# Optimization experiments

Hardware: AMD Instinct MI355X
Metric: run time of the kernel (lower is better)

The kernel has to match this reference:

```python
import jax, jax.numpy as jnp
import numpy as np

N_EVENTS = 16384   # original pixel events
D = 128            # input_size
H = 128            # hidden_size
K = 9              # kernel 3x3 -> patch coords
S = 2048           # number of patch sequences
LMAX = 108         # max sequence length
T = 147456         # total patch events = sum(lengths) = 9 * N_EVENTS


def setup_inputs() -> dict:
    key = jax.random.key(0)
    ks = jax.random.split(key, 8)
    events = jax.random.normal(ks[0], (N_EVENTS, D), jnp.float32)
    pos_id = jax.random.randint(ks[1], (T,), 0, K, dtype=jnp.int32)
    orig_event_idx = jax.random.randint(ks[2], (T,), 0, N_EVENTS, dtype=jnp.int32)
    # alternating 36/108 lengths: 1024*36 + 1024*108 = 147456 = T
    lengths = jnp.where(jnp.arange(S) % 2 == 0, 36, 108).astype(jnp.int32)
    std = float(np.sqrt(2.0 / (D + H)))
    scatter_w = jax.random.normal(ks[3], (K, H, D), jnp.float32) * std
    gather_w = jax.random.normal(ks[4], (K, H, H), jnp.float32) * std
    lstm_std = float(1.0 / np.sqrt(H))
    w_ih = jax.random.uniform(ks[5], (4 * H, H), jnp.float32, -lstm_std, lstm_std)
    w_hh = jax.random.uniform(ks[6], (4 * H, H), jnp.float32, -lstm_std, lstm_std)
    ln_g = jnp.ones((H,), jnp.float32)
    ln_b = jnp.zeros((H,), jnp.float32)
    return dict(events=events, scatter_w=scatter_w, gather_w=gather_w,
                w_ih=w_ih, w_hh=w_hh, ln_g=ln_g, ln_b=ln_b,
                pos_id=pos_id, orig_event_idx=orig_event_idx, lengths=lengths)


def _pos_proj(x, W, pos_id):
    # position-indexed projection: out[t] = W[pos_id[t]] @ x[t]
    # loop over small fixed K=9 with masked accumulate (matches the torch loop)
    out = jnp.zeros((x.shape[0], W.shape[1]), x.dtype)
    for k in range(W.shape[0]):
        out = out + jnp.where((pos_id == k)[:, None], x @ W[k].T, 0.0)
    return out


def reference(events, scatter_w, gather_w, w_ih, w_hh, ln_g, ln_b,
              pos_id, orig_event_idx, lengths):
    # scatter events to patch replicas
    x = events[orig_event_idx]                           # [T, D]
    x = _pos_proj(x, scatter_w, pos_id)                  # [T, H]

    # flat (sequence-major) -> padded [S, LMAX, H]
    seq_offsets = jnp.cumsum(lengths) - lengths          # [S]
    seq_ids = jnp.repeat(jnp.arange(S), lengths, total_repeat_length=T)
    pos_in_seq = jnp.arange(T) - seq_offsets[seq_ids]
    padded = jnp.zeros((S, LMAX, H), x.dtype).at[seq_ids, pos_in_seq].set(x)

    # single-layer bias-free LSTM (pytorch gate order i, f, g, o), zero init.
    # zero-padding after each sequence's valid region leaves valid outputs
    # identical to a PackedSequence LSTM.
    def step(carry, xt):                                 # xt: [S, H]
        h, c = carry
        gates = xt @ w_ih.T + h @ w_hh.T                 # [S, 4H]
        i, f, g, o = jnp.split(gates, 4, axis=-1)
        c = jax.nn.sigmoid(f) * c + jax.nn.sigmoid(i) * jnp.tanh(g)
        h = jax.nn.sigmoid(o) * jnp.tanh(c)
        return (h, c), h

    init = (jnp.zeros((S, H), x.dtype), jnp.zeros((S, H), x.dtype))
    _, hs = jax.lax.scan(step, init, jnp.swapaxes(padded, 0, 1))  # [LMAX, S, H]
    o_flat = jnp.swapaxes(hs, 0, 1)[seq_ids, pos_in_seq]          # [T, H]

    o_flat = _pos_proj(o_flat, gather_w, pos_id)                  # [T, H]

    # gather patch events back to pixel events (scatter-add) + residual + LN
    out = jnp.zeros((N_EVENTS, H), x.dtype).at[orig_event_idx].add(o_flat)
    out = out + events                                   # input_proj is None (D == H)
    mu = jnp.mean(out, axis=-1, keepdims=True)
    var = jnp.var(out, axis=-1, keepdims=True)
    out = (out - mu) * jax.lax.rsqrt(var + 1e-5) * ln_g + ln_b
    return out
```

## Files before the change

### kernel.cpp

```cpp
#include <hip/hip_runtime.h>

#define N_EVENTS 16384
#define DIM 128
#define NK 9
#define NSEQ 2048
#define TT 147456
#define CHUNK 64
#define NCHUNK_MAX (TT/CHUNK + NK)
#define NHBLK 576

typedef __attribute__((ext_vector_type(8))) short bf16x8;
typedef __attribute__((ext_vector_type(4))) float f32x4;
typedef __attribute__((ext_vector_type(4))) int i32x4;
typedef __attribute__((ext_vector_type(2))) int i32x2;

#define OFF_EV     0UL
#define OFF_WC     (OFF_EV   + (size_t)N_EVENTS*DIM*2)
#define OFF_SCAT   (OFF_WC   + (size_t)512*256*2)
#define OFF_GATH   (OFF_SCAT + (size_t)NK*DIM*DIM*2)
#define OFF_XS     (OFF_GATH + (size_t)NK*DIM*DIM*2)
#define OFF_HS     (OFF_XS   + (size_t)TT*DIM*2)
#define OFF_KLIST  (OFF_HS   + (size_t)TT*DIM*2)
#define OFF_ECNT   (OFF_KLIST+ (size_t)TT*4)
#define OFF_EOFF   (OFF_ECNT + 16384UL*4)
#define OFF_ECNT2  (OFF_EOFF + 16392UL*4)
#define OFF_TPOS   (OFF_ECNT2+ 16384UL*4)
#define OFF_SEQOFF (OFF_TPOS + (size_t)TT*4)
#define OFF_GROUP  (OFF_SEQOFF + (size_t)NSEQ*4)
#define OFF_MISC   (OFF_GROUP  + (size_t)NSEQ*4)
#define OFF_BH     (OFF_MISC   + 256UL)

__device__ __forceinline__ short f2b(float f) {
    union { float f; unsigned u; } v; v.f = f;
    unsigned r = (v.u + 0x7FFFu + ((v.u >> 16) & 1u)) >> 16;
    return (short)r;
}
__device__ __forceinline__ float asf(unsigned u) {
    union { unsigned u; float f; } v; v.u = u; return v.f;
}
__device__ __forceinline__ float fsig(float x) {
    return __builtin_amdgcn_rcpf(1.f + __expf(-x));
}
__device__ __forceinline__ float ftanh(float x) {
    return 1.f - 2.f * __builtin_amdgcn_rcpf(__expf(2.f * x) + 1.f);
}

__device__ __forceinline__ float plo(float a, float b) {
    i32x2 r = __builtin_amdgcn_permlane32_swap(__float_as_int(a), __float_as_int(b),
                                               false, false);
    return __int_as_float(r[0]);
}
__device__ __forceinline__ float phi(float a, float b) {
    i32x2 r = __builtin_amdgcn_permlane32_swap(__float_as_int(a), __float_as_int(b),
                                               false, false);
    return __int_as_float(r[1]);
}

__device__ __forceinline__ void mfma_vab(f32x4& c, bf16x8 a, bf16x8 b) {
    asm("v_mfma_f32_16x16x32_bf16 %0, %1, %2, %0" : "+v"(c) : "v"(a), "a"(b));
}
#define MFA(c, a, b) mfma_vab(c, a, b);

__device__ __forceinline__ void wg_bar_nodrain() {
    __builtin_amdgcn_sched_barrier(0);
    asm volatile("s_waitcnt lgkmcnt(0)");
    __builtin_amdgcn_s_barrier();
    __builtin_amdgcn_sched_barrier(0);
}

__global__ void convert_kernel(const float* __restrict__ ev, const float* __restrict__ wih,
                               const float* __restrict__ whh, const float* __restrict__ sw,
                               const float* __restrict__ gw,
                               short* __restrict__ evb, short* __restrict__ wcb,
                               short* __restrict__ swb, short* __restrict__ gwb,
                               int* __restrict__ ecnt, int* __restrict__ ecnt2) {
    int idx = blockIdx.x * blockDim.x + threadIdx.x;
    if (idx < N_EVENTS * DIM) evb[idx] = f2b(ev[idx]);
    if (idx < 512 * DIM) {
        int j = idx >> 7, d = idx & 127;
        wcb[j * 256 + d]       = f2b(wih[idx]);
        wcb[j * 256 + 128 + d] = f2b(whh[idx]);
    }
    if (idx < NK * DIM * DIM) { swb[idx] = f2b(sw[idx]); gwb[idx] = f2b(gw[idx]); }
    if (idx < N_EVENTS) { ecnt[idx] = 0; ecnt2[idx] = 0; }
}

__global__ void hist_kernel(const int* __restrict__ pos, const int* __restrict__ orig,
                            int* __restrict__ blockhist, int* __restrict__ ecnt) {
    __shared__ int h[NK];
    int tid = threadIdx.x;
    if (tid < NK) h[tid] = 0;
    __syncthreads();
    int t = blockIdx.x * 256 + tid;
    atomicAdd(&h[pos[t]], 1);
    atomicAdd(&ecnt[orig[t]], 1);
    __syncthreads();
    if (tid < NK) blockhist[blockIdx.x * NK + tid] = h[tid];
}

__global__ void plan_kernel(int* __restrict__ blockhist, int* __restrict__ misc,
                            const int* __restrict__ lengths, int* __restrict__ seq_off,
                            int* __restrict__ grouped,
                            const int* __restrict__ ecnt, int* __restrict__ eoff) {
    int tid = threadIdx.x;
    if (blockIdx.x == 0) {
        __shared__ int h[NHBLK * NK];
        for (int i = tid; i < NHBLK * NK; i += 256) h[i] = blockhist[i];
        __syncthreads();
        if (tid < NK) {
            int run = 0;
            for (int b = 0; b < NHBLK; b++) {
                int v = h[b * NK + tid];
                h[b * NK + tid] = run;
                run += v;
            }
            misc[tid] = run;
        }
        __syncthreads();
        if (tid == 0) {
            int ko = 0, co = 0;
            for (int k = 0; k < NK; k++) {
                int c = misc[k];
                misc[32 + k] = ko;
                misc[48 + k] = co;
                ko += c;
                co += (c + CHUNK - 1) / CHUNK;
            }
            misc[48 + NK] = co;
        }
        __syncthreads();
        for (int i = tid; i < NHBLK * NK; i += 256) blockhist[i] = h[i];
    } else if (blockIdx.x == 1) {
        __shared__ int lens[NSEQ];
        __shared__ int tsum[256], tlong[256];
        for (int i = tid; i < NSEQ; i += 256) lens[i] = lengths[i];
        __syncthreads();
        int base = tid * 8;
        int ls[8]; int s = 0, lc = 0;
        #pragma unroll
        for (int i = 0; i < 8; i++) { ls[i] = lens[base + i]; s += ls[i]; lc += (ls[i] > 64) ? 1 : 0; }
        tsum[tid] = s; tlong[tid] = lc;
        __syncthreads();
        for (int d = 1; d < 256; d <<= 1) {
            int a = (tid >= d) ? tsum[tid - d] : 0;
            int b = (tid >= d) ? tlong[tid - d] : 0;
            __syncthreads();
            tsum[tid] += a; tlong[tid] += b;
            __syncthreads();
        }
        int nlong_total = tlong[255];
        int excl = tsum[tid] - s;
        int excl_long = tlong[tid] - lc;
        int run = 0, runl = 0;
        #pragma unroll
        for (int i = 0; i < 8; i++) {
            int sid = base + i;
            seq_off[sid] = excl + run;
            int lb = excl_long + runl;
            if (ls[i] > 64) { grouped[lb] = sid; runl++; }
            else            { grouped[nlong_total + (sid - lb)] = sid; }
            run += ls[i];
        }
    } else {
        __shared__ int part[256];
        int base = tid * 64;
        int s = 0;
        for (int j = 0; j < 64; j++) s += ecnt[base + j];
        part[tid] = s;
        __syncthreads();
        for (int d = 1; d < 256; d <<= 1) {
            int a = (tid >= d) ? part[tid - d] : 0;
            __syncthreads();
            part[tid] += a;
            __syncthreads();
        }
        int run = part[tid] - s;
        for (int j = 0; j < 64; j++) {
            eoff[base + j] = run;
            run += ecnt[base + j];
        }
        if (tid == 255) eoff[N_EVENTS] = run;
    }
}

__global__ void fill_kernel(const int* __restrict__ pos, const int* __restrict__ orig,
                            const int* __restrict__ blockhist, const int* __restrict__ misc,
                            int* __restrict__ klist,
                            const int* __restrict__ eoff, int* __restrict__ ecnt2,
                            int* __restrict__ tokpos) {
    __shared__ int off[NK];
    int tid = threadIdx.x;
    if (tid < NK) off[tid] = misc[32 + tid] + blockhist[blockIdx.x * NK + tid];
    __syncthreads();
    int t = blockIdx.x * 256 + tid;
    int p = atomicAdd(&off[pos[t]], 1);
    klist[p] = t;
    int o = orig[t];
    int p2 = atomicAdd(&ecnt2[o], 1);
    tokpos[t] = eoff[o] + p2;
}

__global__ void bucket_gemm(const short* __restrict__ src, const short* __restrict__ wall,
                            const int* __restrict__ klist, const int* __restrict__ misc,
                            const int* __restrict__ orig, const int* __restrict__ tokpos,
                            short* __restrict__ rows_out, int mode) {
    const int* chunkoff = misc + 48;
    int b = blockIdx.x;
    if (b >= chunkoff[NK]) return;
    int k = 0;
    while (k < NK - 1 && chunkoff[k + 1] <= b) k++;
    int lc = b - chunkoff[k];
    int cnt = misc[k];
    int base = misc[32 + k] + lc * CHUNK;
    int nv = min(CHUNK, cnt - lc * CHUNK);

    __shared__ int wpos[CHUNK], ridx[CHUNK];
    __shared__ short A[CHUNK * 136];
    int tid = threadIdx.x;
    if (tid < CHUNK) {
        int tv = klist[base + ((tid < nv) ? tid : 0)];
        ridx[tid] = (mode == 0) ? orig[tv] : tv;
        wpos[tid] = (mode == 0) ? tv : tokpos[tv];
    }
    __syncthreads();
    {
        int row = tid >> 2, part = tid & 3;
        const i32x4* s4 = (const i32x4*)(src + (size_t)ridx[row] * DIM + part * 32);
        i32x4* d4 = (i32x4*)(A + row * 136 + part * 32);
        d4[0] = s4[0]; d4[1] = s4[1]; d4[2] = s4[2]; d4[3] = s4[3];
    }
    __syncthreads();
    int wave = tid >> 6, lane = tid & 63, l15 = lane & 15, q = lane >> 4;
    const short* wk = wall + (size_t)k * DIM * DIM;
    bf16x8 Bf[2][4];
    #pragma unroll
    for (int nt = 0; nt < 2; nt++) {
        int h = wave * 32 + nt * 16 + l15;
        #pragma unroll
        for (int kt = 0; kt < 4; kt++)
            Bf[nt][kt] = *(const bf16x8*)(wk + h * DIM + kt * 32 + q * 8);
    }
    f32x4 C[4][2];
    #pragma unroll
    for (int mt = 0; mt < 4; mt++)
        #pragma unroll
        for (int nt = 0; nt < 2; nt++) C[mt][nt] = (f32x4){0.f, 0.f, 0.f, 0.f};
    #pragma unroll
    for (int mt = 0; mt < 4; mt++) {
        bf16x8 Afr[4];
        const short* ar = A + (mt * 16 + l15) * 136 + q * 8;
        Afr[0] = *(const bf16x8*)(ar);
        Afr[1] = *(const bf16x8*)(ar + 32);
        Afr[2] = *(const bf16x8*)(ar + 64);
        Afr[3] = *(const bf16x8*)(ar + 96);
        #pragma unroll
        for (int nt = 0; nt < 2; nt++)
            #pragma unroll
            for (int kt = 0; kt < 4; kt++)
                C[mt][nt] = __builtin_amdgcn_mfma_f32_16x16x32_bf16(Afr[kt], Bf[nt][kt], C[mt][nt], 0, 0, 0);
    }
    __syncthreads();
    #pragma unroll
    for (int mt = 0; mt < 4; mt++)
        #pragma unroll
        for (int nt = 0; nt < 2; nt++)
            #pragma unroll
            for (int r = 0; r < 4; r++) {
                int row = mt * 16 + q * 4 + r;
                int col = wave * 32 + nt * 16 + l15;
                A[row * 136 + col] = f2b(C[mt][nt][r]);
            }
    __syncthreads();
    {
        int row = tid >> 2, part = tid & 3;
        if (row < nv) {
            const i32x4* s4 = (const i32x4*)(A + row * 136 + part * 32);
            i32x4* d4 = (i32x4*)(rows_out + (size_t)wpos[row] * DIM + part * 32);
            d4[0] = s4[0]; d4[1] = s4[1]; d4[2] = s4[2]; d4[3] = s4[3];
        }
    }
}

#define TAIL(IDX, SEL, SLOT) { \
    float iA = SEL(Ci[0], Ci[2]), iB = SEL(Ci[1], Ci[3]); \
    float fA = SEL(Cf[0], Cf[2]), fB = SEL(Cf[1], Cf[3]); \
    float gA = SEL(Cg[0], Cg[2]), gB = SEL(Cg[1], Cg[3]); \
    float oA = SEL(Co[0], Co[2]), oB = SEL(Co[1], Co[3]); \
    if ((IDX) < lenA) { \
        float si = fsig(iA), sf = fsig(fA), so = fsig(oA); \
        float tg = ftanh(gA); \
        float cn = sf * cA + si * tg; \
        float th = ftanh(cn); \
        cA = cn; \
        hb[(SLOT) * 1088 + rowA * 136 + u] = f2b(so * th); \
    } \
    if ((IDX) < lenB) { \
        float si = fsig(iB), sf = fsig(fB), so = fsig(oB); \
        float tg = ftanh(gB); \
        float cn = sf * cB + si * tg; \
        float th = ftanh(cn); \
        cB = cn; \
        hb[(SLOT) * 1088 + rowB * 136 + u] = f2b(so * th); \
    } \
}

#define LSTM_G(J2, PF) { \
    const int i2 = ib8 + 2 * (J2); \
    f32x4 Ci = {0.f,0.f,0.f,0.f}, Cf = {0.f,0.f,0.f,0.f}; \
    f32x4 Cg = {0.f,0.f,0.f,0.f}, Co = {0.f,0.f,0.f,0.f}; \
    MFA(Ci, PF[0], Bf[0][0]) MFA(Cf, PF[0], Bf[1][0]) \
    MFA(Cg, PF[0], Bf[2][0]) MFA(Co, PF[0], Bf[3][0]) \
    MFA(Ci, PF[1], Bf[0][1]) MFA(Cf, PF[1], Bf[1][1]) \
    MFA(Cg, PF[1], Bf[2][1]) MFA(Co, PF[1], Bf[3][1]) \
    MFA(Ci, PF[2], Bf[0][2]) MFA(Cf, PF[2], Bf[1][2]) \
    MFA(Cg, PF[2], Bf[2][2]) MFA(Co, PF[2], Bf[3][2]) \
    MFA(Ci, PF[3], Bf[0][3]) MFA(Cf, PF[3], Bf[1][3]) \
    MFA(Cg, PF[3], Bf[2][3]) MFA(Co, PF[3], Bf[3][3]) \
    bf16x8 He0, He1, He2, He3; \
    { const short* hp_ = b0 + (lo8 ? (((2*(J2)+7)&7) * 1088) : 8704); \
      He0 = *(const bf16x8*)(hp_);      He1 = *(const bf16x8*)(hp_ + 32); \
      He2 = *(const bf16x8*)(hp_ + 64); He3 = *(const bf16x8*)(hp_ + 96); } \
    MFA(Ci, He0, Bf[0][4]) MFA(Cf, He0, Bf[1][4]) \
    MFA(Cg, He0, Bf[2][4]) MFA(Co, He0, Bf[3][4]) \
    MFA(Ci, He1, Bf[0][5]) MFA(Cf, He1, Bf[1][5]) \
    MFA(Cg, He1, Bf[2][5]) MFA(Co, He1, Bf[3][5]) \
    MFA(Ci, He2, Bf[0][6]) MFA(Cf, He2, Bf[1][6]) \
    MFA(Cg, He2, Bf[2][6]) MFA(Co, He2, Bf[3][6]) \
    MFA(Ci, He3, Bf[0][7]) MFA(Cf, He3, Bf[1][7]) \
    MFA(Cg, He3, Bf[2][7]) MFA(Co, He3, Bf[3][7]) \
    TAIL(i2, plo, (2*(J2)) & 7) \
    wg_bar_nodrain(); \
    bf16x8 Ho0, Ho1, Ho2, Ho3; \
    { const short* hp_ = b0 + (lo8 ? 8704 : (((2*(J2)) & 7) * 1088)); \
      Ho0 = *(const bf16x8*)(hp_);      Ho1 = *(const bf16x8*)(hp_ + 32); \
      Ho2 = *(const bf16x8*)(hp_ + 64); Ho3 = *(const bf16x8*)(hp_ + 96); } \
    MFA(Ci, Ho0, Bf[0][4]) MFA(Cf, Ho0, Bf[1][4]) \
    MFA(Cg, Ho0, Bf[2][4]) MFA(Co, Ho0, Bf[3][4]) \
    MFA(Ci, Ho1, Bf[0][5]) MFA(Cf, Ho1, Bf[1][5]) \
    MFA(Cg, Ho1, Bf[2][5]) MFA(Co, Ho1, Bf[3][5]) \
    MFA(Ci, Ho2, Bf[0][6]) MFA(Cf, Ho2, Bf[1][6]) \
    MFA(Cg, Ho2, Bf[2][6]) MFA(Co, Ho2, Bf[3][6]) \
    MFA(Ci, Ho3, Bf[0][7]) MFA(Cf, Ho3, Bf[1][7]) \
    MFA(Cg, Ho3, Bf[2][7]) MFA(Co, Ho3, Bf[3][7]) \
    { const short* xp_ = xs + xoff; \
      PF[0] = *(const bf16x8*)(xp_);      PF[1] = *(const bf16x8*)(xp_ + 32); \
      PF[2] = *(const bf16x8*)(xp_ + 64); PF[3] = *(const bf16x8*)(xp_ + 96); } \
    xoff += ((i2 + 6 + loff) < my_len) ? 2 * DIM : 0; \
    TAIL(i2 + 1, phi, (2*(J2)+1) & 7) \
    wg_bar_nodrain(); \
}

__global__ __launch_bounds__(512)
__attribute__((amdgpu_waves_per_eu(2, 2)))
void lstm_kernel(
        const short* __restrict__ xs, const short* __restrict__ wc,
        short* __restrict__ hstore, const int* __restrict__ seq_off,
        const int* __restrict__ grouped, const int* __restrict__ lengths) {
    __shared__ int s_off[8], s_len[8];
    __shared__ short hchunk[11][8][136];
    int tid = threadIdx.x;
    if (tid < 8) {
        int s = grouped[blockIdx.x * 8 + tid];
        s_off[tid] = seq_off[s];
        s_len[tid] = lengths[s];
    }
    for (int j = tid; j < 11 * 8 * 136; j += 512) ((short*)hchunk)[j] = 0;
    __syncthreads();
    int lane = tid & 63, l15 = lane & 15, ql = lane >> 4;
    int wave = tid >> 6;
    int u = wave * 16 + l15;
    short* hb = (short*)hchunk;
    bf16x8 Bf[4][8];
    #pragma unroll
    for (int g = 0; g < 4; g++) {
        int j = g * 128 + u;
        #pragma unroll
        for (int kt = 0; kt < 8; kt++)
            Bf[g][kt] = *(const bf16x8*)(wc + j * 256 + kt * 32 + ql * 8);
    }
    int maxlen = 0;
    #pragma unroll
    for (int i = 0; i < 8; i++) maxlen = max(maxlen, s_len[i]);
    int sq = l15 & 7;
    int loff = l15 >> 3;
    bool lo8 = (l15 < 8);
    int my_off = s_off[sq];
    int my_len = s_len[sq];
    const short* b0 = hb + sq * 136 + ql * 8;
    int rowA = (ql < 2) ? (ql * 4 + 0) : ((ql - 2) * 4 + 2);
    int rowB = (ql < 2) ? (ql * 4 + 1) : ((ql - 2) * 4 + 3);
    int lenA = s_len[rowA], lenB = s_len[rowB];
    float cA = 0.f, cB = 0.f;
    bf16x8 Pf0[4], Pf1[4];
    int xoff = (my_off + loff) * DIM + ql * 8;
    {
        const short* xp = xs + xoff;
        Pf0[0] = *(const bf16x8*)(xp);      Pf0[1] = *(const bf16x8*)(xp + 32);
        Pf0[2] = *(const bf16x8*)(xp + 64); Pf0[3] = *(const bf16x8*)(xp + 96);
        const short* xq = xp + 2 * DIM;
        Pf1[0] = *(const bf16x8*)(xq);      Pf1[1] = *(const bf16x8*)(xq + 32);
        Pf1[2] = *(const bf16x8*)(xq + 64); Pf1[3] = *(const bf16x8*)(xq + 96);
    }
    xoff += 4 * DIM;

    int nb8 = (maxlen + 7) >> 3;
    for (int ob = 0; ob < nb8; ob++) {
        int ib8 = ob * 8;
        LSTM_G(0, Pf0)
        LSTM_G(1, Pf1)
        LSTM_G(2, Pf0)
        LSTM_G(3, Pf1)
        #pragma unroll
        for (int it = 0; it < 2; it++) {
            int idx = tid + it * 512;
            int st = idx >> 7, s = (idx >> 4) & 7, part = idx & 15;
            int ig = ib8 + st;
            if (ig < s_len[s]) {
                i32x4 v = *(const i32x4*)&hchunk[st][s][part * 8];
                *(i32x4*)(hstore + (size_t)(s_off[s] + ig) * DIM + part * 8) = v;
            }
        }
        wg_bar_nodrain();
    }
}

__global__ void gather_ln(const short* __restrict__ of, const int* __restrict__ eoff,
                          const float* __restrict__ ev,
                          const float* __restrict__ g, const float* __restrict__ bta,
                          float* __restrict__ out) {
    int tid = threadIdx.x;
    int wave = tid >> 6, lane = tid & 63;
    int e = blockIdx.x * 4 + wave;
    int s0 = eoff[e], s1 = eoff[e + 1];
    float x0 = 0.f, x1 = 0.f;
    for (int j = s0; j < s1; j++) {
        unsigned v = *(const unsigned*)(of + (size_t)j * DIM + lane * 2);
        x0 += asf(v << 16);
        x1 += asf(v & 0xffff0000u);
    }
    const float2* e2 = (const float2*)(ev + (size_t)e * DIM);
    float2 evv = e2[lane];
    x0 += evv.x; x1 += evv.y;
    float sm = x0 + x1, sq = x0 * x0 + x1 * x1;
    #pragma unroll
    for (int m = 1; m < 64; m <<= 1) {
        sm += __shfl_xor(sm, m, 64);
        sq += __shfl_xor(sq, m, 64);
    }
    float mean = sm * (1.f / DIM);
    float var = sq * (1.f / DIM) - mean * mean;
    float rs = rsqrtf(var + 1e-5f);
    float2 gv = ((const float2*)g)[lane], bv = ((const float2*)bta)[lane];
    float2 ov;
    ov.x = (x0 - mean) * rs * gv.x + bv.x;
    ov.y = (x1 - mean) * rs * gv.y + bv.y;
    ((float2*)(out + (size_t)e * DIM))[lane] = ov;
}

extern "C" void kernel_launch(void* const* d_in, const int* in_sizes, int n_in,
                              void* d_out, int out_size, void* d_ws, size_t ws_size,
                              hipStream_t stream) {
    const float* events = (const float*)d_in[0];
    const float* scat   = (const float*)d_in[1];
    const float* gath   = (const float*)d_in[2];
    const float* wih    = (const float*)d_in[3];
    const float* whh    = (const float*)d_in[4];
    const float* lng    = (const float*)d_in[5];
    const float* lnb    = (const float*)d_in[6];
    const int* posid    = (const int*)d_in[7];
    const int* orig     = (const int*)d_in[8];
    const int* lens     = (const int*)d_in[9];
    char* ws = (char*)d_ws;
    short* evb   = (short*)(ws + OFF_EV);
    short* wcb   = (short*)(ws + OFF_WC);
    short* swb   = (short*)(ws + OFF_SCAT);
    short* gwb   = (short*)(ws + OFF_GATH);
    short* xs    = (short*)(ws + OFF_XS);
    short* hs    = (short*)(ws + OFF_HS);
    int*   klist = (int*)(ws + OFF_KLIST);
    int*   ecnt  = (int*)(ws + OFF_ECNT);
    int*   eoff  = (int*)(ws + OFF_EOFF);
    int*   ecnt2 = (int*)(ws + OFF_ECNT2);
    int*   tpos  = (int*)(ws + OFF_TPOS);
    int*   seqo  = (int*)(ws + OFF_SEQOFF);
    int*   grp   = (int*)(ws + OFF_GROUP);
    int*   misc  = (int*)(ws + OFF_MISC);
    int*   bh    = (int*)(ws + OFF_BH);
    float* out   = (float*)d_out;

    convert_kernel<<<8192, 256, 0, stream>>>(events, wih, whh, scat, gath,
                                             evb, wcb, swb, gwb, ecnt, ecnt2);
    hist_kernel<<<NHBLK, 256, 0, stream>>>(posid, orig, bh, ecnt);
    plan_kernel<<<3, 256, 0, stream>>>(bh, misc, lens, seqo, grp, ecnt, eoff);
    fill_kernel<<<NHBLK, 256, 0, stream>>>(posid, orig, bh, misc, klist, eoff, ecnt2, tpos);
    bucket_gemm<<<NCHUNK_MAX, 256, 0, stream>>>(evb, swb, klist, misc, orig, tpos, xs, 0);
    lstm_kernel<<<256, 512, 0, stream>>>(xs, wcb, hs, seqo, grp, lens);
    bucket_gemm<<<NCHUNK_MAX, 256, 0, stream>>>(hs, gwb, klist, misc, orig, tpos, xs, 1);
    gather_ln<<<4096, 256, 0, stream>>>(xs, eoff, events, lng, lnb, out);
}
```

Measured before the change: 281.4 us.

## Enlarge bucket GEMM chunk to 128 rows with 512 threads and precomputed index lists

The bucketed position-projection GEMM now handles 128 rows per block with 8 waves, each wave owning a 16-column slice of the weight, and the weight fragment loads are hoisted ahead of the row gather. The fill kernel now writes per-bucket source and destination index arrays, so the GEMM reads them contiguously instead of doing a two-level indirection through klist and orig/tokpos. This is meant to amortise weight loads and dependent index lookups over more rows. In exchange each block uses more LDS, and there are fewer blocks, which can reduce occupancy and increase wasted work in partially filled chunks.

New measurement: 285.7 us. Within noise of the previous version (+1.5%).

```diff
diff --git a/kernel.cpp b/kernel.cpp
--- a/kernel.cpp
+++ b/kernel.cpp
@@ -5,7 +5,7 @@
 #define NK 9
 #define NSEQ 2048
 #define TT 147456
-#define CHUNK 64
+#define CHUNK 128
 #define NCHUNK_MAX (TT/CHUNK + NK)
 #define NHBLK 576
 
@@ -24,8 +24,9 @@
 #define OFF_ECNT   (OFF_KLIST+ (size_t)TT*4)
 #define OFF_EOFF   (OFF_ECNT + 16384UL*4)
 #define OFF_ECNT2  (OFF_EOFF + 16392UL*4)
-#define OFF_TPOS   (OFF_ECNT2+ 16384UL*4)
-#define OFF_SEQOFF (OFF_TPOS + (size_t)TT*4)
+#define OFF_KSRC   (OFF_ECNT2+ 16384UL*4)
+#define OFF_KDST   (OFF_KSRC + (size_t)TT*4)
+#define OFF_SEQOFF (OFF_KDST + (size_t)TT*4)
 #define OFF_GROUP  (OFF_SEQOFF + (size_t)NSEQ*4)
 #define OFF_MISC   (OFF_GROUP  + (size_t)NSEQ*4)
 #define OFF_BH     (OFF_MISC   + 256UL)
@@ -187,7 +188,7 @@
                             const int* __restrict__ blockhist, const int* __restrict__ misc,
                             int* __restrict__ klist,
                             const int* __restrict__ eoff, int* __restrict__ ecnt2,
-                            int* __restrict__ tokpos) {
+                            int* __restrict__ ksrc0, int* __restrict__ kdst1) {
     __shared__ int off[NK];
     int tid = threadIdx.x;
     if (tid < NK) off[tid] = misc[32 + tid] + blockhist[blockIdx.x * NK + tid];
@@ -197,13 +198,15 @@
     klist[p] = t;
     int o = orig[t];
     int p2 = atomicAdd(&ecnt2[o], 1);
-    tokpos[t] = eoff[o] + p2;
-}
-
-__global__ void bucket_gemm(const short* __restrict__ src, const short* __restrict__ wall,
-                            const int* __restrict__ klist, const int* __restrict__ misc,
-                            const int* __restrict__ orig, const int* __restrict__ tokpos,
-                            short* __restrict__ rows_out, int mode) {
+    ksrc0[p] = o;
+    kdst1[p] = eoff[o] + p2;
+}
+
+__global__ __launch_bounds__(512) void bucket_gemm(
+        const short* __restrict__ src, const short* __restrict__ wall,
+        const int* __restrict__ klist, const int* __restrict__ misc,
+        const int* __restrict__ ksrc0, const int* __restrict__ kdst1,
+        short* __restrict__ rows_out, int mode) {
     const int* chunkoff = misc + 48;
     int b = blockIdx.x;
     if (b >= chunkoff[NK]) return;
@@ -214,13 +217,21 @@
     int base = misc[32 + k] + lc * CHUNK;
     int nv = min(CHUNK, cnt - lc * CHUNK);
 
+    int tid = threadIdx.x;
+    int wave = tid >> 6, lane = tid & 63, l15 = lane & 15, q = lane >> 4;
+    const short* wk = wall + (size_t)k * DIM * DIM;
+    int h = wave * 16 + l15;
+    bf16x8 Bf[4];
+    #pragma unroll
+    for (int kt = 0; kt < 4; kt++)
+        Bf[kt] = *(const bf16x8*)(wk + h * DIM + kt * 32 + q * 8);
+
     __shared__ int wpos[CHUNK], ridx[CHUNK];
     __shared__ short A[CHUNK * 136];
-    int tid = threadIdx.x;
     if (tid < CHUNK) {
-        int tv = klist[base + ((tid < nv) ? tid : 0)];
-        ridx[tid] = (mode == 0) ? orig[tv] : tv;
-        wpos[tid] = (mode == 0) ? tv : tokpos[tv];
+        int idx = base + ((tid < nv) ? tid : 0);
+        if (mode == 0) { ridx[tid] = ksrc0[idx]; wpos[tid] = klist[idx]; }
+        else           { ridx[tid] = klist[idx]; wpos[tid] = kdst1[idx]; }
     }
     __syncthreads();
     {
@@ -230,23 +241,11 @@
         d4[0] = s4[0]; d4[1] = s4[1]; d4[2] = s4[2]; d4[3] = s4[3];
     }
     __syncthreads();
-    int wave = tid >> 6, lane = tid & 63, l15 = lane & 15, q = lane >> 4;
-    const short* wk = wall + (size_t)k * DIM * DIM;
-    bf16x8 Bf[2][4];
-    #pragma unroll
-    for (int nt = 0; nt < 2; nt++) {
-        int h = wave * 32 + nt * 16 + l15;
-        #pragma unroll
-        for (int kt = 0; kt < 4; kt++)
-            Bf[nt][kt] = *(const bf16x8*)(wk + h * DIM + kt * 32 + q * 8);
-    }
-    f32x4 C[4][2];
-    #pragma unroll
-    for (int mt = 0; mt < 4; mt++)
-        #pragma unroll
-        for (int nt = 0; nt < 2; nt++) C[mt][nt] = (f32x4){0.f, 0.f, 0.f, 0.f};
-    #pragma unroll
-    for (int mt = 0; mt < 4; mt++) {
+    f32x4 C[8];
+    #pragma unroll
+    for (int mt = 0; mt < 8; mt++) C[mt] = (f32x4){0.f, 0.f, 0.f, 0.f};
+    #pragma unroll
+    for (int mt = 0; mt < 8; mt++) {
         bf16x8 Afr[4];
         const short* ar = A + (mt * 16 + l15) * 136 + q * 8;
         Afr[0] = *(const bf16x8*)(ar);
@@ -254,22 +253,18 @@
         Afr[2] = *(const bf16x8*)(ar + 64);
         Afr[3] = *(const bf16x8*)(ar + 96);
         #pragma unroll
-        for (int nt = 0; nt < 2; nt++)
-            #pragma unroll
-            for (int kt = 0; kt < 4; kt++)
-                C[mt][nt] = __builtin_amdgcn_mfma_f32_16x16x32_bf16(Afr[kt], Bf[nt][kt], C[mt][nt], 0, 0, 0);
-    }
-    __syncthreads();
-    #pragma unroll
-    for (int mt = 0; mt < 4; mt++)
-        #pragma unroll
-        for (int nt = 0; nt < 2; nt++)
-            #pragma unroll
-            for (int r = 0; r < 4; r++) {
-                int row = mt * 16 + q * 4 + r;
-                int col = wave * 32 + nt * 16 + l15;
-                A[row * 136 + col] = f2b(C[mt][nt][r]);
-            }
+        for (int kt = 0; kt < 4; kt++)
+            C[mt] = __builtin_amdgcn_mfma_f32_16x16x32_bf16(Afr[kt], Bf[kt], C[mt], 0, 0, 0);
+    }
+    __syncthreads();
+    #pragma unroll
+    for (int mt = 0; mt < 8; mt++)
+        #pragma unroll
+        for (int r = 0; r < 4; r++) {
+            int row = mt * 16 + q * 4 + r;
+            int col = wave * 16 + l15;
+            A[row * 136 + col] = f2b(C[mt][r]);
+        }
     __syncthreads();
     {
         int row = tid >> 2, part = tid & 3;
@@ -481,7 +476,8 @@
     int*   ecnt  = (int*)(ws + OFF_ECNT);
     int*   eoff  = (int*)(ws + OFF_EOFF);
     int*   ecnt2 = (int*)(ws + OFF_ECNT2);
-    int*   tpos  = (int*)(ws + OFF_TPOS);
+    int*   ksrc0 = (int*)(ws + OFF_KSRC);
+    int*   kdst1 = (int*)(ws + OFF_KDST);
     int*   seqo  = (int*)(ws + OFF_SEQOFF);
     int*   grp   = (int*)(ws + OFF_GROUP);
     int*   misc  = (int*)(ws + OFF_MISC);
@@ -492,9 +488,10 @@
                                              evb, wcb, swb, gwb, ecnt, ecnt2);
     hist_kernel<<<NHBLK, 256, 0, stream>>>(posid, orig, bh, ecnt);
     plan_kernel<<<3, 256, 0, stream>>>(bh, misc, lens, seqo, grp, ecnt, eoff);
-    fill_kernel<<<NHBLK, 256, 0, stream>>>(posid, orig, bh, misc, klist, eoff, ecnt2, tpos);
-    bucket_gemm<<<NCHUNK_MAX, 256, 0, stream>>>(evb, swb, klist, misc, orig, tpos, xs, 0);
+    fill_kernel<<<NHBLK, 256, 0, stream>>>(posid, orig, bh, misc, klist, eoff, ecnt2,
+                                           ksrc0, kdst1);
+    bucket_gemm<<<NCHUNK_MAX, 512, 0, stream>>>(evb, swb, klist, misc, ksrc0, kdst1, xs, 0);
     lstm_kernel<<<256, 512, 0, stream>>>(xs, wcb, hs, seqo, grp, lens);
-    bucket_gemm<<<NCHUNK_MAX, 256, 0, stream>>>(hs, gwb, klist, misc, orig, tpos, xs, 1);
+    bucket_gemm<<<NCHUNK_MAX, 512, 0, stream>>>(hs, gwb, klist, misc, ksrc0, kdst1, xs, 1);
     gather_ln<<<4096, 256, 0, stream>>>(xs, eoff, events, lng, lnb, out);
 }
```

## Fuse convert and position histogram kernels; build event histogram in plan block LDS

Applied to the files above, without the earlier changes.

Merges the bf16 conversion kernel and the position histogram kernel into one grid-stride launch with NHBLK blocks, which removes a kernel launch and the global ecnt zeroing. The per-event count histogram moves out of global atomics and into one plan_kernel block, which now scans all 147456 orig indices with shared-memory atomics. That saves global atomic traffic, but it puts a serial 147K-element loop on a single workgroup, which could lengthen the plan stage's critical path.

Result: slower. 412.8 us (+46.7%).

```diff
diff --git a/kernel.cpp b/kernel.cpp
--- a/kernel.cpp
+++ b/kernel.cpp
@@ -68,43 +68,44 @@
     __builtin_amdgcn_sched_barrier(0);
 }
 
-__global__ void convert_kernel(const float* __restrict__ ev, const float* __restrict__ wih,
-                               const float* __restrict__ whh, const float* __restrict__ sw,
-                               const float* __restrict__ gw,
-                               short* __restrict__ evb, short* __restrict__ wcb,
-                               short* __restrict__ swb, short* __restrict__ gwb,
-                               int* __restrict__ ecnt, int* __restrict__ ecnt2) {
-    int idx = blockIdx.x * blockDim.x + threadIdx.x;
-    if (idx < N_EVENTS * DIM) evb[idx] = f2b(ev[idx]);
-    if (idx < 512 * DIM) {
+__global__ __launch_bounds__(256) void convhist_kernel(
+        const float* __restrict__ ev, const float* __restrict__ wih,
+        const float* __restrict__ whh, const float* __restrict__ sw,
+        const float* __restrict__ gw,
+        short* __restrict__ evb, short* __restrict__ wcb,
+        short* __restrict__ swb, short* __restrict__ gwb,
+        int* __restrict__ ecnt2,
+        const int* __restrict__ pos, int* __restrict__ blockhist) {
+    __shared__ int h[NK];
+    int tid = threadIdx.x;
+    int b = blockIdx.x;
+    int gidx = b * 256 + tid;
+    const int GSTRIDE = NHBLK * 256;
+    if (tid < NK) h[tid] = 0;
+    __syncthreads();
+    atomicAdd(&h[pos[gidx]], 1);
+    for (int idx = gidx; idx < N_EVENTS * DIM; idx += GSTRIDE) evb[idx] = f2b(ev[idx]);
+    for (int idx = gidx; idx < 512 * DIM; idx += GSTRIDE) {
         int j = idx >> 7, d = idx & 127;
         wcb[j * 256 + d]       = f2b(wih[idx]);
         wcb[j * 256 + 128 + d] = f2b(whh[idx]);
     }
-    if (idx < NK * DIM * DIM) { swb[idx] = f2b(sw[idx]); gwb[idx] = f2b(gw[idx]); }
-    if (idx < N_EVENTS) { ecnt[idx] = 0; ecnt2[idx] = 0; }
-}
-
-__global__ void hist_kernel(const int* __restrict__ pos, const int* __restrict__ orig,
-                            int* __restrict__ blockhist, int* __restrict__ ecnt) {
-    __shared__ int h[NK];
-    int tid = threadIdx.x;
-    if (tid < NK) h[tid] = 0;
-    __syncthreads();
-    int t = blockIdx.x * 256 + tid;
-    atomicAdd(&h[pos[t]], 1);
-    atomicAdd(&ecnt[orig[t]], 1);
-    __syncthreads();
-    if (tid < NK) blockhist[blockIdx.x * NK + tid] = h[tid];
+    for (int idx = gidx; idx < NK * DIM * DIM; idx += GSTRIDE) {
+        swb[idx] = f2b(sw[idx]); gwb[idx] = f2b(gw[idx]);
+    }
+    for (int idx = gidx; idx < N_EVENTS; idx += GSTRIDE) ecnt2[idx] = 0;
+    __syncthreads();
+    if (tid < NK) blockhist[b * NK + tid] = h[tid];
 }
 
 __global__ void plan_kernel(int* __restrict__ blockhist, int* __restrict__ misc,
                             const int* __restrict__ lengths, int* __restrict__ seq_off,
                             int* __restrict__ grouped,
-                            const int* __restrict__ ecnt, int* __restrict__ eoff) {
+                            const int* __restrict__ orig, int* __restrict__ eoff) {
+    __shared__ int smem[N_EVENTS + 256];
     int tid = threadIdx.x;
     if (blockIdx.x == 0) {
-        __shared__ int h[NHBLK * NK];
+        int* h = smem;
         for (int i = tid; i < NHBLK * NK; i += 256) h[i] = blockhist[i];
         __syncthreads();
         if (tid < NK) {
@@ -131,8 +132,9 @@
         __syncthreads();
         for (int i = tid; i < NHBLK * NK; i += 256) blockhist[i] = h[i];
     } else if (blockIdx.x == 1) {
-        __shared__ int lens[NSEQ];
-        __shared__ int tsum[256], tlong[256];
+        int* lens = smem;
+        int* tsum = smem + 2048;
+        int* tlong = smem + 2304;
         for (int i = tid; i < NSEQ; i += 256) lens[i] = lengths[i];
         __syncthreads();
         int base = tid * 8;
@@ -162,10 +164,15 @@
             run += ls[i];
         }
     } else {
-        __shared__ int part[256];
+        int* hist = smem;
+        int* part = smem + N_EVENTS;
+        for (int i = tid; i < N_EVENTS; i += 256) hist[i] = 0;
+        __syncthreads();
+        for (int i = tid; i < TT; i += 256) atomicAdd(&hist[orig[i]], 1);
+        __syncthreads();
         int base = tid * 64;
         int s = 0;
-        for (int j = 0; j < 64; j++) s += ecnt[base + j];
+        for (int j = 0; j < 64; j++) s += hist[base + j];
         part[tid] = s;
         __syncthreads();
         for (int d = 1; d < 256; d <<= 1) {
@@ -177,7 +184,7 @@
         int run = part[tid] - s;
         for (int j = 0; j < 64; j++) {
             eoff[base + j] = run;
-            run += ecnt[base + j];
+            run += hist[base + j];
         }
         if (tid == 255) eoff[N_EVENTS] = run;
     }
@@ -478,7 +485,6 @@
     short* xs    = (short*)(ws + OFF_XS);
     short* hs    = (short*)(ws + OFF_HS);
     int*   klist = (int*)(ws + OFF_KLIST);
-    int*   ecnt  = (int*)(ws + OFF_ECNT);
     int*   eoff  = (int*)(ws + OFF_EOFF);
     int*   ecnt2 = (int*)(ws + OFF_ECNT2);
     int*   tpos  = (int*)(ws + OFF_TPOS);
@@ -488,10 +494,9 @@
     int*   bh    = (int*)(ws + OFF_BH);
     float* out   = (float*)d_out;
 
-    convert_kernel<<<8192, 256, 0, stream>>>(events, wih, whh, scat, gath,
-                                             evb, wcb, swb, gwb, ecnt, ecnt2);
-    hist_kernel<<<NHBLK, 256, 0, stream>>>(posid, orig, bh, ecnt);
-    plan_kernel<<<3, 256, 0, stream>>>(bh, misc, lens, seqo, grp, ecnt, eoff);
+    convhist_kernel<<<NHBLK, 256, 0, stream>>>(events, wih, whh, scat, gath,
+                                               evb, wcb, swb, gwb, ecnt2, posid, bh);
+    plan_kernel<<<3, 256, 0, stream>>>(bh, misc, lens, seqo, grp, orig, eoff);
     fill_kernel<<<NHBLK, 256, 0, stream>>>(posid, orig, bh, misc, klist, eoff, ecnt2, tpos);
     bucket_gemm<<<NCHUNK_MAX, 256, 0, stream>>>(evb, swb, klist, misc, orig, tpos, xs, 0);
     lstm_kernel<<<256, 512, 0, stream>>>(xs, wcb, hs, seqo, grp, lens);
```
